# Kernel tuning notes

Hardware: AMD Instinct MI355X
Metric: run time of the kernel (lower is better)

Reference implementation:

```python
import jax, jax.numpy as jnp
import numpy as np

R, B, D, C = 64, 4096, 512, 128  # n_rules, batch, n_fea, n_cls


def setup_inputs() -> dict:
    key = jax.random.key(0)
    k0, k1, k2, k3, k4 = jax.random.split(key, 5)
    x = jax.random.normal(k0, (B, D), dtype=jnp.float32)
    proto = jax.random.normal(k1, (R, D), dtype=jnp.float32)
    var = jax.random.uniform(k2, (R, D), dtype=jnp.float32)
    W = jax.random.normal(k3, (R, D, C), dtype=jnp.float32) * 0.02
    b = jax.random.normal(k4, (R, C), dtype=jnp.float32) * 0.02
    return {"x": x, "proto": proto, "var": var, "W": W, "b": b}


def reference(x, proto, var, W, b):
    # Antecedent: Gaussian membership per rule, var clamped to [1e-4, 0.1]
    v = jnp.clip(var, 0.0001, 0.1)                                  # [R, D]
    diff = x[None, :, :] - proto[:, None, :]                        # [R, B, D]
    m = jnp.exp(-diff * diff / (2.0 * v[:, None, :] ** 2))          # [R, B, D]
    # Firing strength: sum of squared memberships over features, softmax over rules
    fs_ini = jnp.sum(m * m, axis=-1).T                              # [B, R]
    fire_strength = jax.nn.softmax(fs_ini, axis=1)                  # [B, R]
    # Consequent: per-rule Linear + ReLU (batched GEMM over rules)
    expert = jax.nn.relu(jnp.einsum('bd,rdc->rbc', x, W) + b[:, None, :])  # [R, B, C]
    # Softmax-weighted combine over rules
    out = jnp.einsum('rbc,br->bc', expert, fire_strength)           # [B, C]
    return out, fire_strength
```

## Files before the change

### kernel.cpp

```cpp
#include <hip/hip_runtime.h>
#include <hip/hip_bf16.h>
#include <cmath>

#define R_ 64
#define B_ 4096
#define D_ 512
#define C_ 128

typedef __attribute__((ext_vector_type(8))) short bf16x8;
typedef __attribute__((ext_vector_type(4))) float f32x4;

__device__ __forceinline__ unsigned short f2bf(float f) {
  union { float f; unsigned u; } x; x.f = f;
  unsigned r = (x.u + 0x7FFFu + ((x.u >> 16) & 1u)) >> 16;
  return (unsigned short)r;
}

__global__ void prep_x_kernel(const float* __restrict__ x, unsigned short* __restrict__ xw) {
  int i = blockIdx.x * 256 + threadIdx.x;
  float4 v = reinterpret_cast<const float4*>(x)[i];
  ushort4 o;
  o.x = f2bf(v.x); o.y = f2bf(v.y); o.z = f2bf(v.z); o.w = f2bf(v.w);
  reinterpret_cast<ushort4*>(xw)[i] = o;
}

__global__ void prep_w_kernel(const float* __restrict__ W, unsigned short* __restrict__ wt) {
  __shared__ float t[32][33];
  int bx = blockIdx.x;
  int r = bx >> 6;
  int rem = bx & 63;
  int d0 = (rem >> 2) << 5;
  int c0 = (rem & 3) << 5;
  int tx = threadIdx.x & 31, ty = threadIdx.x >> 5;
  const float* Wr = W + (size_t)r * D_ * C_;
#pragma unroll
  for (int q = 0; q < 4; ++q) {
    int dl = q * 8 + ty;
    t[dl][tx] = Wr[(size_t)(d0 + dl) * C_ + c0 + tx];
  }
  __syncthreads();
  unsigned short* wtr = wt + (size_t)r * C_ * D_;
#pragma unroll
  for (int q = 0; q < 4; ++q) {
    int cl = q * 8 + ty;
    float v = t[tx][cl];
    wtr[(size_t)(c0 + cl) * D_ + d0 + tx] = f2bf(v);
  }
}

__global__ void prep_ps_kernel(const float* __restrict__ proto, const float* __restrict__ var,
                               float* __restrict__ ps) {
  int i = blockIdx.x * 256 + threadIdx.x;
  float v = fminf(fmaxf(var[i], 1e-4f), 0.1f);
  float s = 1.2011224087864498f / v;
  float2 o; o.x = s; o.y = -proto[i] * s;
  reinterpret_cast<float2*>(ps)[i] = o;
}

__global__ __launch_bounds__(256, 4) void fs_partial_kernel(
    const float* __restrict__ x, const float* __restrict__ ps,
    float* __restrict__ fire) {
  __shared__ float x_s[16 * 68];
  __shared__ __align__(16) float ps_s[64 * 128];
  const int tid = threadIdx.x;
  const int b0 = blockIdx.x * 16;
  const int dq = blockIdx.y;

  {
    int row = tid >> 4, c4 = tid & 15;
    float4 v = *reinterpret_cast<const float4*>(&x[(size_t)(b0 + row) * D_ + dq * 64 + c4 * 4]);
    *reinterpret_cast<float4*>(&x_s[row * 68 + c4 * 4]) = v;
  }
#pragma unroll
  for (int k = 0; k < 8; ++k) {
    int g = tid + k * 256;
    int row = g >> 5, gi = g & 31;
    float4 v = *reinterpret_cast<const float4*>(&ps[(size_t)row * (D_ * 2) + dq * 128 + gi * 4]);
    int gs = gi ^ (row & 31);
    *reinterpret_cast<float4*>((char*)ps_s + row * 512 + (gs << 4)) = v;
  }
  __syncthreads();

  const int tr = tid & 63;
  const int tb = tid >> 6;
  const int s31 = tr & 31;
  const char* pb = (const char*)ps_s + tr * 512;
  float facc[4] = {0.f, 0.f, 0.f, 0.f};

#pragma unroll
  for (int d4 = 0; d4 < 16; ++d4) {
    float4 psa = *reinterpret_cast<const float4*>(pb + ((((d4 * 2) ^ s31)) << 4));
    float4 psb = *reinterpret_cast<const float4*>(pb + ((((d4 * 2 + 1) ^ s31)) << 4));
#pragma unroll
    for (int i = 0; i < 4; ++i) {
      float4 xv = *reinterpret_cast<const float4*>(&x_s[(tb * 4 + i) * 68 + d4 * 4]);
      float u0 = fmaf(xv.x, psa.x, psa.y);
      float u1 = fmaf(xv.y, psa.z, psa.w);
      float u2 = fmaf(xv.z, psb.x, psb.y);
      float u3 = fmaf(xv.w, psb.z, psb.w);
      facc[i] += exp2f(-(u0 * u0)) + exp2f(-(u1 * u1)) +
                 exp2f(-(u2 * u2)) + exp2f(-(u3 * u3));
    }
  }
#pragma unroll
  for (int i = 0; i < 4; ++i)
    atomicAdd(&fire[(size_t)(b0 + tb * 4 + i) * R_ + tr], facc[i]);
}

__global__ void softmax_kernel(float* __restrict__ fire) {
  const int b = blockIdx.x * 4 + (threadIdx.x >> 6);
  const int r = threadIdx.x & 63;
  float v = fire[(size_t)b * R_ + r];
  float m = v;
#pragma unroll
  for (int off = 32; off; off >>= 1) m = fmaxf(m, __shfl_xor(m, off, 64));
  float e = exp2f((v - m) * 1.4426950408889634f);
  float s = e;
#pragma unroll
  for (int off = 32; off; off >>= 1) s += __shfl_xor(s, off, 64);
  fire[(size_t)b * R_ + r] = e / s;
}

__global__ __launch_bounds__(512, 2) void gemm_kernel(
    const unsigned short* __restrict__ xw, const unsigned short* __restrict__ wt,
    const float* __restrict__ fire, const float* __restrict__ bias,
    float* __restrict__ out) {
  __shared__ __align__(16) unsigned short x_s[2][128 * 64];
  __shared__ __align__(16) unsigned short w_s[2][128 * 64];
  __shared__ float fire_s[128 * 8];
  __shared__ float bias_s[8 * 128];

  const int tid = threadIdx.x;
  const int bm = blockIdx.x;
  const int rg = blockIdx.y;
  const int b0 = bm * 128;

  {
    int t = tid;
#pragma unroll
    for (int q = 0; q < 2; ++q, t += 512) {
      int row = t >> 3, g = t & 7;
      fire_s[t] = fire[(size_t)(b0 + row) * R_ + rg * 8 + g];
    }
    t = tid;
#pragma unroll
    for (int q = 0; q < 2; ++q, t += 512) {
      bias_s[t] = bias[rg * 8 * C_ + t];
    }
  }

  const int wid = tid >> 6, lane = tid & 63;
  const int wm = wid >> 2, wn = wid & 3;
  const int l16 = lane & 15, lhi = lane >> 4;

  int offA[4][2], offB[2][2];
#pragma unroll
  for (int m = 0; m < 4; ++m) {
    int row = wm * 64 + m * 16 + l16;
#pragma unroll
    for (int ks = 0; ks < 2; ++ks)
      offA[m][ks] = row * 128 + (((ks * 4 + lhi) ^ (row & 7)) << 4);
  }
#pragma unroll
  for (int n = 0; n < 2; ++n) {
    int row = wn * 32 + n * 16 + l16;
#pragma unroll
    for (int ks = 0; ks < 2; ++ks)
      offB[n][ks] = row * 128 + (((ks * 4 + lhi) ^ (row & 7)) << 4);
  }

  const unsigned short* xsrc = xw + (size_t)b0 * D_;

  float tot[4][2][4];
#pragma unroll
  for (int m = 0; m < 4; ++m)
#pragma unroll
    for (int n = 0; n < 2; ++n)
#pragma unroll
      for (int j = 0; j < 4; ++j) tot[m][n][j] = 0.f;

  f32x4 acc[4][2];

  auto stage = [&](unsigned short* lds, const unsigned short* src, int kc) {
#pragma unroll
    for (int t2 = 0; t2 < 2; ++t2) {
      int ch = t2 * 512 + tid;
      int row = ch >> 3, g = ch & 7;
      const unsigned short* ga = src + (size_t)row * D_ + kc + ((g ^ (row & 7)) << 3);
      __builtin_amdgcn_global_load_lds(
          (const __attribute__((address_space(1))) void*)ga,
          (__attribute__((address_space(3))) void*)(lds + ch * 8), 16, 0, 0);
    }
  };

  stage(x_s[0], xsrc, 0);
  stage(w_s[0], wt + (size_t)(rg * 8) * C_ * D_, 0);
  asm volatile("s_waitcnt vmcnt(0)" ::: "memory");
  __syncthreads();

  int cur = 0;
  for (int s = 0; s < 64; ++s) {
    const int g = s >> 3, kk = s & 7;
    if (kk == 0) {
#pragma unroll
      for (int m = 0; m < 4; ++m)
#pragma unroll
        for (int n = 0; n < 2; ++n)
          acc[m][n] = f32x4{0.f, 0.f, 0.f, 0.f};
    }
    if (s + 1 < 64) {
      const int s1 = s + 1;
      stage(x_s[cur ^ 1], xsrc, (s1 & 7) * 64);
      stage(w_s[cur ^ 1], wt + (size_t)(rg * 8 + (s1 >> 3)) * C_ * D_, (s1 & 7) * 64);
    }
    const char* xb = (const char*)x_s[cur];
    const char* wb = (const char*)w_s[cur];
    bf16x8 av[4][2], bv[2][2];
#pragma unroll
    for (int m = 0; m < 4; ++m)
#pragma unroll
      for (int ks = 0; ks < 2; ++ks)
        av[m][ks] = *reinterpret_cast<const bf16x8*>(xb + offA[m][ks]);
#pragma unroll
    for (int n = 0; n < 2; ++n)
#pragma unroll
      for (int ks = 0; ks < 2; ++ks)
        bv[n][ks] = *reinterpret_cast<const bf16x8*>(wb + offB[n][ks]);
#pragma unroll
    for (int ks = 0; ks < 2; ++ks)
#pragma unroll
      for (int m = 0; m < 4; ++m)
#pragma unroll
        for (int n = 0; n < 2; ++n)
          acc[m][n] = __builtin_amdgcn_mfma_f32_16x16x32_bf16(av[m][ks], bv[n][ks], acc[m][n], 0, 0, 0);
    if (kk == 7) {
#pragma unroll
      for (int m = 0; m < 4; ++m)
#pragma unroll
        for (int n = 0; n < 2; ++n) {
          int col = wn * 32 + n * 16 + l16;
          float bi = bias_s[g * 128 + col];
#pragma unroll
          for (int j = 0; j < 4; ++j) {
            int rowl = wm * 64 + m * 16 + lhi * 4 + j;
            float v = acc[m][n][j] + bi;
            v = fmaxf(v, 0.f);
            tot[m][n][j] += v * fire_s[rowl * 8 + g];
          }
        }
    }
    asm volatile("s_waitcnt vmcnt(0)" ::: "memory");
    __syncthreads();
    cur ^= 1;
  }

#pragma unroll
  for (int m = 0; m < 4; ++m)
#pragma unroll
    for (int n = 0; n < 2; ++n) {
      int col = wn * 32 + n * 16 + l16;
#pragma unroll
      for (int j = 0; j < 4; ++j) {
        int rowl = wm * 64 + m * 16 + lhi * 4 + j;
        atomicAdd(&out[(size_t)(b0 + rowl) * C_ + col], tot[m][n][j]);
      }
    }
}

extern "C" void kernel_launch(void* const* d_in, const int* in_sizes, int n_in,
                              void* d_out, int out_size, void* d_ws, size_t ws_size,
                              hipStream_t stream) {
  const float* x     = (const float*)d_in[0];
  const float* proto = (const float*)d_in[1];
  const float* var   = (const float*)d_in[2];
  const float* W     = (const float*)d_in[3];
  const float* bias  = (const float*)d_in[4];
  float* out  = (float*)d_out;
  float* fire = out + (size_t)B_ * C_;

  const size_t WS_X  = (size_t)B_ * D_ * sizeof(unsigned short);
  const size_t WS_WT = (size_t)R_ * C_ * D_ * sizeof(unsigned short);
  const size_t WS_PS = (size_t)R_ * D_ * 2 * sizeof(float);
  if (ws_size < WS_X + WS_WT + WS_PS) return;

  unsigned short* xw  = (unsigned short*)d_ws;
  unsigned short* wtp = (unsigned short*)((char*)d_ws + WS_X);
  float*          ps  = (float*)((char*)d_ws + WS_X + WS_WT);

  hipMemsetAsync(d_out, 0, (size_t)out_size * sizeof(float), stream);
  prep_x_kernel<<<dim3((B_ * D_ / 4) / 256), dim3(256), 0, stream>>>(x, xw);
  prep_w_kernel<<<dim3(R_ * 64), dim3(256), 0, stream>>>(W, wtp);
  prep_ps_kernel<<<dim3(R_ * D_ / 256), dim3(256), 0, stream>>>(proto, var, ps);
  fs_partial_kernel<<<dim3(B_ / 16, 8), dim3(256), 0, stream>>>(x, ps, fire);
  softmax_kernel<<<dim3(B_ / 4), dim3(256), 0, stream>>>(fire);
  gemm_kernel<<<dim3(B_ / 128, R_ / 8), dim3(512), 0, stream>>>(xw, wtp, fire, bias, out);
}
```

Measured before the change: 133.1 us.

## Fuse bf16 x conversion into fs kernel and split GEMM over more rule groups

Removes the separate x-to-bf16 prep kernel by writing the bf16 copy of x from the tile already staged in shared memory by the firing-strength kernel. The GEMM now covers 4 rules per block instead of 8, doubling the grid to 512 blocks. Block indices are remapped so that blocks sharing rule groups land on the same XCD, and occupancy is raised via launch_bounds. Staging switches from direct global-to-LDS loads to register-staged loads written to LDS after the compute, overlapping the fetch with the MFMAs. This costs more atomics on the output and more register pressure.

```diff
diff --git a/kernel.cpp b/kernel.cpp
--- a/kernel.cpp
+++ b/kernel.cpp
@@ -14,14 +14,6 @@
   union { float f; unsigned u; } x; x.f = f;
   unsigned r = (x.u + 0x7FFFu + ((x.u >> 16) & 1u)) >> 16;
   return (unsigned short)r;
-}
-
-__global__ void prep_x_kernel(const float* __restrict__ x, unsigned short* __restrict__ xw) {
-  int i = blockIdx.x * 256 + threadIdx.x;
-  float4 v = reinterpret_cast<const float4*>(x)[i];
-  ushort4 o;
-  o.x = f2bf(v.x); o.y = f2bf(v.y); o.z = f2bf(v.z); o.w = f2bf(v.w);
-  reinterpret_cast<ushort4*>(xw)[i] = o;
 }
 
 __global__ void prep_w_kernel(const float* __restrict__ W, unsigned short* __restrict__ wt) {
@@ -59,7 +51,7 @@
 
 __global__ __launch_bounds__(256, 4) void fs_partial_kernel(
     const float* __restrict__ x, const float* __restrict__ ps,
-    float* __restrict__ fire) {
+    float* __restrict__ fire, unsigned short* __restrict__ xw) {
   __shared__ float x_s[16 * 68];
   __shared__ __align__(16) float ps_s[64 * 128];
   const int tid = threadIdx.x;
@@ -80,6 +72,14 @@
     *reinterpret_cast<float4*>((char*)ps_s + row * 512 + (gs << 4)) = v;
   }
   __syncthreads();
+
+  {
+    int row = tid >> 4, c0 = (tid & 15) * 4;
+    const float* sp = &x_s[row * 68 + c0];
+    ushort4 o;
+    o.x = f2bf(sp[0]); o.y = f2bf(sp[1]); o.z = f2bf(sp[2]); o.w = f2bf(sp[3]);
+    *reinterpret_cast<ushort4*>(&xw[(size_t)(b0 + row) * D_ + dq * 64 + c0]) = o;
+  }
 
   const int tr = tid & 63;
   const int tb = tid >> 6;
@@ -121,32 +121,27 @@
   fire[(size_t)b * R_ + r] = e / s;
 }
 
-__global__ __launch_bounds__(512, 2) void gemm_kernel(
+__global__ __launch_bounds__(512, 4) void gemm_kernel(
     const unsigned short* __restrict__ xw, const unsigned short* __restrict__ wt,
     const float* __restrict__ fire, const float* __restrict__ bias,
     float* __restrict__ out) {
   __shared__ __align__(16) unsigned short x_s[2][128 * 64];
   __shared__ __align__(16) unsigned short w_s[2][128 * 64];
-  __shared__ float fire_s[128 * 8];
-  __shared__ float bias_s[8 * 128];
+  __shared__ float fire_s[128 * 4];
+  __shared__ float bias_s[4 * 128];
 
   const int tid = threadIdx.x;
-  const int bm = blockIdx.x;
-  const int rg = blockIdx.y;
+  const int f = blockIdx.x;
+  const int xcd = f & 7;
+  const int idx = f >> 3;
+  const int rg = 2 * xcd + (idx & 1);
+  const int bm = idx >> 1;
   const int b0 = bm * 128;
 
   {
-    int t = tid;
-#pragma unroll
-    for (int q = 0; q < 2; ++q, t += 512) {
-      int row = t >> 3, g = t & 7;
-      fire_s[t] = fire[(size_t)(b0 + row) * R_ + rg * 8 + g];
-    }
-    t = tid;
-#pragma unroll
-    for (int q = 0; q < 2; ++q, t += 512) {
-      bias_s[t] = bias[rg * 8 * C_ + t];
-    }
+    int row = tid >> 2, g = tid & 3;
+    fire_s[tid] = fire[(size_t)(b0 + row) * R_ + rg * 4 + g];
+    bias_s[tid] = bias[rg * 4 * C_ + tid];
   }
 
   const int wid = tid >> 6, lane = tid & 63;
@@ -169,7 +164,19 @@
       offB[n][ks] = row * 128 + (((ks * 4 + lhi) ^ (row & 7)) << 4);
   }
 
+  int a_goff[2], a_ldst[2], b_goff[2], b_ldst[2];
+#pragma unroll
+  for (int q = 0; q < 2; ++q) {
+    int ch = q * 512 + tid;
+    int row = ch >> 3, g = ch & 7;
+    a_goff[q] = row * D_ + g * 8;
+    a_ldst[q] = row * 128 + ((g ^ (row & 7)) << 4);
+    b_goff[q] = row * D_ + g * 8;
+    b_ldst[q] = row * 128 + ((g ^ (row & 7)) << 4);
+  }
+
   const unsigned short* xsrc = xw + (size_t)b0 * D_;
+  const unsigned short* wbase = wt + (size_t)(rg * 4) * C_ * D_;
 
   float tot[4][2][4];
 #pragma unroll
@@ -181,25 +188,23 @@
 
   f32x4 acc[4][2];
 
-  auto stage = [&](unsigned short* lds, const unsigned short* src, int kc) {
-#pragma unroll
-    for (int t2 = 0; t2 < 2; ++t2) {
-      int ch = t2 * 512 + tid;
-      int row = ch >> 3, g = ch & 7;
-      const unsigned short* ga = src + (size_t)row * D_ + kc + ((g ^ (row & 7)) << 3);
-      __builtin_amdgcn_global_load_lds(
-          (const __attribute__((address_space(1))) void*)ga,
-          (__attribute__((address_space(3))) void*)(lds + ch * 8), 16, 0, 0);
-    }
-  };
-
-  stage(x_s[0], xsrc, 0);
-  stage(w_s[0], wt + (size_t)(rg * 8) * C_ * D_, 0);
-  asm volatile("s_waitcnt vmcnt(0)" ::: "memory");
+  {
+    uint4 la[2], lb[2];
+#pragma unroll
+    for (int q = 0; q < 2; ++q) {
+      la[q] = *reinterpret_cast<const uint4*>(xsrc + a_goff[q]);
+      lb[q] = *reinterpret_cast<const uint4*>(wbase + b_goff[q]);
+    }
+#pragma unroll
+    for (int q = 0; q < 2; ++q) {
+      *reinterpret_cast<uint4*>((char*)x_s[0] + a_ldst[q]) = la[q];
+      *reinterpret_cast<uint4*>((char*)w_s[0] + b_ldst[q]) = lb[q];
+    }
+  }
   __syncthreads();
 
   int cur = 0;
-  for (int s = 0; s < 64; ++s) {
+  for (int s = 0; s < 32; ++s) {
     const int g = s >> 3, kk = s & 7;
     if (kk == 0) {
 #pragma unroll
@@ -208,31 +213,34 @@
         for (int n = 0; n < 2; ++n)
           acc[m][n] = f32x4{0.f, 0.f, 0.f, 0.f};
     }
-    if (s + 1 < 64) {
+    uint4 la[2], lb[2];
+    if (s + 1 < 32) {
       const int s1 = s + 1;
-      stage(x_s[cur ^ 1], xsrc, (s1 & 7) * 64);
-      stage(w_s[cur ^ 1], wt + (size_t)(rg * 8 + (s1 >> 3)) * C_ * D_, (s1 & 7) * 64);
+      const unsigned short* xs1 = xsrc + (s1 & 7) * 64;
+      const unsigned short* ws1 = wbase + (size_t)(s1 >> 3) * C_ * D_ + (s1 & 7) * 64;
+#pragma unroll
+      for (int q = 0; q < 2; ++q) {
+        la[q] = *reinterpret_cast<const uint4*>(xs1 + a_goff[q]);
+        lb[q] = *reinterpret_cast<const uint4*>(ws1 + b_goff[q]);
+      }
     }
     const char* xb = (const char*)x_s[cur];
     const char* wb = (const char*)w_s[cur];
-    bf16x8 av[4][2], bv[2][2];
-#pragma unroll
-    for (int m = 0; m < 4; ++m)
-#pragma unroll
-      for (int ks = 0; ks < 2; ++ks)
-        av[m][ks] = *reinterpret_cast<const bf16x8*>(xb + offA[m][ks]);
-#pragma unroll
-    for (int n = 0; n < 2; ++n)
-#pragma unroll
-      for (int ks = 0; ks < 2; ++ks)
-        bv[n][ks] = *reinterpret_cast<const bf16x8*>(wb + offB[n][ks]);
-#pragma unroll
-    for (int ks = 0; ks < 2; ++ks)
+#pragma unroll
+    for (int ks = 0; ks < 2; ++ks) {
+      bf16x8 av[4], bv[2];
 #pragma unroll
       for (int m = 0; m < 4; ++m)
+        av[m] = *reinterpret_cast<const bf16x8*>(xb + offA[m][ks]);
+#pragma unroll
+      for (int n = 0; n < 2; ++n)
+        bv[n] = *reinterpret_cast<const bf16x8*>(wb + offB[n][ks]);
+#pragma unroll
+      for (int m = 0; m < 4; ++m)
 #pragma unroll
         for (int n = 0; n < 2; ++n)
-          acc[m][n] = __builtin_amdgcn_mfma_f32_16x16x32_bf16(av[m][ks], bv[n][ks], acc[m][n], 0, 0, 0);
+          acc[m][n] = __builtin_amdgcn_mfma_f32_16x16x32_bf16(av[m], bv[n], acc[m][n], 0, 0, 0);
+    }
     if (kk == 7) {
 #pragma unroll
       for (int m = 0; m < 4; ++m)
@@ -245,11 +253,17 @@
             int rowl = wm * 64 + m * 16 + lhi * 4 + j;
             float v = acc[m][n][j] + bi;
             v = fmaxf(v, 0.f);
-            tot[m][n][j] += v * fire_s[rowl * 8 + g];
+            tot[m][n][j] += v * fire_s[rowl * 4 + g];
           }
         }
     }
-    asm volatile("s_waitcnt vmcnt(0)" ::: "memory");
+    if (s + 1 < 32) {
+#pragma unroll
+      for (int q = 0; q < 2; ++q) {
+        *reinterpret_cast<uint4*>((char*)x_s[cur ^ 1] + a_ldst[q]) = la[q];
+        *reinterpret_cast<uint4*>((char*)w_s[cur ^ 1] + b_ldst[q]) = lb[q];
+      }
+    }
     __syncthreads();
     cur ^= 1;
   }
@@ -288,10 +302,9 @@
   float*          ps  = (float*)((char*)d_ws + WS_X + WS_WT);
 
   hipMemsetAsync(d_out, 0, (size_t)out_size * sizeof(float), stream);
-  prep_x_kernel<<<dim3((B_ * D_ / 4) / 256), dim3(256), 0, stream>>>(x, xw);
   prep_w_kernel<<<dim3(R_ * 64), dim3(256), 0, stream>>>(W, wtp);
   prep_ps_kernel<<<dim3(R_ * D_ / 256), dim3(256), 0, stream>>>(proto, var, ps);
-  fs_partial_kernel<<<dim3(B_ / 16, 8), dim3(256), 0, stream>>>(x, ps, fire);
+  fs_partial_kernel<<<dim3(B_ / 16, 8), dim3(256), 0, stream>>>(x, ps, fire, xw);
   softmax_kernel<<<dim3(B_ / 4), dim3(256), 0, stream>>>(fire);
-  gemm_kernel<<<dim3(B_ / 128, R_ / 8), dim3(512), 0, stream>>>(xw, wtp, fire, bias, out);
-}
+  gemm_kernel<<<dim3(512), dim3(512), 0, stream>>>(xw, wtp, fire, bias, out);
+}
```

Result: faster. 114.1 us (-14.3%).
